# Optimization experiments

Measured on AMD Instinct MI355X. Metric: run time of the kernel, lower is better.

Reference implementation:

```python
import jax, jax.numpy as jnp
import numpy as np
import math
from itertools import combinations_with_replacement

D_KEY, D_VAL, P = 32, 64, 2
ALPHA = 1.0 / (math.factorial(P) * D_KEY ** (P / 2))  # 1/(p! * d_key^(p/2))
B, H, S = 1, 8, 512


def _make_M_C():
    # M_p: unique monomial index tuples i_1 <= ... <= i_p, shape [m_p, p]
    M = np.array(list(combinations_with_replacement(range(D_KEY), P)), dtype=np.int32)
    m_p = M.shape[0]
    counts = np.zeros((m_p, D_KEY), dtype=np.int64)
    for j in range(P):
        counts[np.arange(m_p), M[:, j]] += 1
    logfac_counts = np.vectorize(lambda v: math.lgamma(v + 1.0))(counts).sum(-1)
    C = np.round(np.exp(math.lgamma(P + 1.0) - logfac_counts)).astype(np.float32)
    return M, C


def setup_inputs() -> dict:
    key = jax.random.key(0)
    kq, kk, kv = jax.random.split(key, 3)
    M, C = _make_M_C()
    return {
        "Q": jax.random.normal(kq, (B, H, S, D_KEY), dtype=jnp.float32),
        "K": jax.random.normal(kk, (B, H, S, D_KEY), dtype=jnp.float32),
        "V": jax.random.normal(kv, (B, H, S, D_VAL), dtype=jnp.float32),
        "M": jnp.asarray(M),
        "C": jnp.asarray(C),
        "continue_prev": 0,
    }


def reference(Q, K, V, M, C, continue_prev):
    # Monomial features: Phi[b,h,s,m] = prod_j X[b,h,s,M[m,j]]
    Phi_Q = jnp.prod(Q[..., M], axis=-1)  # [B,H,S,m]
    Phi_K = jnp.prod(K[..., M], axis=-1)  # [B,H,S,m]
    # Causal prefix-sum of the Phi_K (x) V outer-product state
    H_S = jnp.cumsum(Phi_K[..., None] * V[..., None, :], axis=-3) * ALPHA  # [B,H,S,m,d_val]
    H_Z = jnp.cumsum(Phi_K, axis=-2) * ALPHA                                # [B,H,S,m] (d=1 squeezed)
    # continue_prev is False (0): no carried state to add.
    Y_S = jnp.einsum('m,bhsm,bhsmd->bhsd', C, Phi_Q, H_S)  # [B,H,S,d_val]
    Y_Z = jnp.einsum('m,bhsm,bhsm->bhs', C, Phi_Q, H_Z)[..., None]  # [B,H,S,1]
    return Y_S, Y_Z
```

## Files before the change

### kernel.cpp

```cpp
#include <hip/hip_runtime.h>
#include <hip/hip_bf16.h>


typedef __attribute__((ext_vector_type(8))) short short8;
typedef __attribute__((ext_vector_type(4))) float floatx4;

constexpr int H_ = 8, S_ = 512, DK = 32, DV = 64;
constexpr float ALPHA = 1.0f / 64.0f;

__device__ __forceinline__ unsigned int pk_bf16(float a, float b) {
    __hip_bfloat162 h = __float22bfloat162_rn(make_float2(a, b));
    union { __hip_bfloat162 h2; unsigned int u; } cvt;
    cvt.h2 = h;
    return cvt.u;
}
__device__ __forceinline__ void split8_cvt(float4 a, float4 b, short8& hi, short8& lo) {
    float f[8] = {a.x, a.y, a.z, a.w, b.x, b.y, b.z, b.w};
    unsigned int hp[4];
    hp[0] = pk_bf16(f[0], f[1]); hp[1] = pk_bf16(f[2], f[3]);
    hp[2] = pk_bf16(f[4], f[5]); hp[3] = pk_bf16(f[6], f[7]);
    float lo_f[8];
    #pragma unroll
    for (int p = 0; p < 4; ++p) {
        float he = __uint_as_float(hp[p] << 16);
        float ho = __uint_as_float(hp[p] & 0xFFFF0000u);
        lo_f[2 * p]     = f[2 * p]     - he;
        lo_f[2 * p + 1] = f[2 * p + 1] - ho;
    }
    unsigned int lp[4];
    lp[0] = pk_bf16(lo_f[0], lo_f[1]); lp[1] = pk_bf16(lo_f[2], lo_f[3]);
    lp[2] = pk_bf16(lo_f[4], lo_f[5]); lp[3] = pk_bf16(lo_f[6], lo_f[7]);
    #pragma unroll
    for (int p = 0; p < 4; ++p) {
        hi[2 * p] = (short)(hp[p] & 0xFFFF); hi[2 * p + 1] = (short)(hp[p] >> 16);
        lo[2 * p] = (short)(lp[p] & 0xFFFF); lo[2 * p + 1] = (short)(lp[p] >> 16);
    }
}

__global__ __launch_bounds__(512) void taylor_fused_v6(
    const float* __restrict__ Qg, const float* __restrict__ Kg,
    const float* __restrict__ Vg, float* __restrict__ out)
{
    const int t = threadIdx.x;
    const int c = t >> 6;
    const int l = t & 63;
    const int h = blockIdx.x & 7;
    const int qt = 15 - (blockIdx.x >> 3);
    const int qbase = qt * 32;
    const int nc = (qt >> 1) + 1;
    const int g = l >> 4, r15 = l & 15;

    __shared__ alignas(16) char Ssm[8 * 4096];
    __shared__ alignas(16) float4 Racc[8][8][64];
    __shared__ float Zb[8][32];

    floatx4 acc[2][4] = {};
    float zacc[2] = {0.f, 0.f};

    if (c < nc) {
        const bool last = (c == nc - 1);

        float4 qraw[2][2];
        #pragma unroll
        for (int qtile = 0; qtile < 2; ++qtile) {
            const float* qp = Qg + (size_t)(h * S_ + qbase + qtile * 16 + r15) * DK + g * 8;
            qraw[qtile][0] = *(const float4*)qp;
            qraw[qtile][1] = *(const float4*)(qp + 4);
        }
        float4 kraw[4][2];
        #pragma unroll
        for (int ktile = 0; ktile < 4; ++ktile) {
            const float* kp = Kg + (size_t)(h * S_ + c * 64 + ktile * 16 + r15) * DK + g * 8;
            kraw[ktile][0] = *(const float4*)kp;
            kraw[ktile][1] = *(const float4*)(kp + 4);
        }
        float vraw[2][4][8];
        #pragma unroll
        for (int kc = 0; kc < 2; ++kc)
            #pragma unroll
            for (int dtile = 0; dtile < 4; ++dtile) {
                const float* vp = Vg + (size_t)(h * S_ + c * 64 + kc * 32 + g * 8) * DV
                                     + dtile * 16 + r15;
                #pragma unroll
                for (int j = 0; j < 8; ++j)
                    vraw[kc][dtile][j] = vp[(size_t)j * DV];
            }

        short8 qBh[2], qBl[2];
        #pragma unroll
        for (int qtile = 0; qtile < 2; ++qtile)
            split8_cvt(qraw[qtile][0], qraw[qtile][1], qBh[qtile], qBl[qtile]);

        char* ssmW = Ssm + c * 4096;

        #pragma unroll
        for (int ktile = 0; ktile < 4; ++ktile) {
            short8 kAh, kAl;
            split8_cvt(kraw[ktile][0], kraw[ktile][1], kAh, kAl);
            #pragma unroll
            for (int qtile = 0; qtile < 2; ++qtile) {
                floatx4 cc_ = {0.f, 0.f, 0.f, 0.f};
                cc_ = __builtin_amdgcn_mfma_f32_16x16x32_bf16(kAh, qBh[qtile], cc_, 0, 0, 0);
                cc_ = __builtin_amdgcn_mfma_f32_16x16x32_bf16(kAh, qBl[qtile], cc_, 0, 0, 0);
                cc_ = __builtin_amdgcn_mfma_f32_16x16x32_bf16(kAl, qBh[qtile], cc_, 0, 0, 0);
                const int qg = qbase + qtile * 16 + r15;
                const int kb = c * 64 + ktile * 16 + g * 4;
                float s[4];
                #pragma unroll
                for (int rr = 0; rr < 4; ++rr) {
                    float sv = cc_[rr] * cc_[rr] * ALPHA;
                    if (last && (kb + rr > qg)) sv = 0.f;
                    s[rr] = sv;
                }
                zacc[qtile] += (s[0] + s[1]) + (s[2] + s[3]);
                unsigned int p0 = pk_bf16(s[0], s[1]);
                unsigned int p1 = pk_bf16(s[2], s[3]);
                const int qrow = qtile * 16 + r15;
                const int k0 = ktile * 16 + g * 4;
                const int byte = qrow * 128 + (((k0 >> 3) ^ (qrow & 7)) << 4) + ((k0 & 7) * 2);
                *(unsigned int*)(ssmW + byte)     = p0;
                *(unsigned int*)(ssmW + byte + 4) = p1;
            }
        }

        short8 vB[2][4];
        #pragma unroll
        for (int kc = 0; kc < 2; ++kc)
            #pragma unroll
            for (int dtile = 0; dtile < 4; ++dtile) {
                #pragma unroll
                for (int p = 0; p < 4; ++p) {
                    unsigned int pk = pk_bf16(vraw[kc][dtile][2 * p], vraw[kc][dtile][2 * p + 1]);
                    vB[kc][dtile][2 * p]     = (short)(pk & 0xFFFF);
                    vB[kc][dtile][2 * p + 1] = (short)(pk >> 16);
                }
            }

        #pragma unroll
        for (int kc = 0; kc < 2; ++kc) {
            short8 sA[2];
            #pragma unroll
            for (int qtile = 0; qtile < 2; ++qtile) {
                const int qrow = qtile * 16 + r15;
                const int g16 = kc * 4 + g;
                sA[qtile] = *(const short8*)(ssmW + qrow * 128 + ((g16 ^ (qrow & 7)) << 4));
            }
            #pragma unroll
            for (int dtile = 0; dtile < 4; ++dtile) {
                acc[0][dtile] = __builtin_amdgcn_mfma_f32_16x16x32_bf16(sA[0], vB[kc][dtile], acc[0][dtile], 0, 0, 0);
                acc[1][dtile] = __builtin_amdgcn_mfma_f32_16x16x32_bf16(sA[1], vB[kc][dtile], acc[1][dtile], 0, 0, 0);
            }
        }

        #pragma unroll
        for (int qtile = 0; qtile < 2; ++qtile) {
            float z = zacc[qtile];
            z += __shfl_xor(z, 16);
            z += __shfl_xor(z, 32);
            zacc[qtile] = z;
        }
    }

    {
        #pragma unroll
        for (int f = 0; f < 8; ++f) {
            floatx4 a = acc[f >> 2][f & 3];
            Racc[c][f][l] = make_float4(a[0], a[1], a[2], a[3]);
        }
        if (l < 32) Zb[c][l] = (l < 16) ? zacc[0] : zacc[1];
    }
    __syncthreads();

    {
        float4 sum = make_float4(0.f, 0.f, 0.f, 0.f);
        #pragma unroll
        for (int cw = 0; cw < 8; ++cw) {
            float4 v = Racc[cw][c][l];
            sum.x += v.x; sum.y += v.y; sum.z += v.z; sum.w += v.w;
        }
        const int qtile = c >> 2, dtile = c & 3;
        const int d = dtile * 16 + r15;
        float sv[4] = {sum.x, sum.y, sum.z, sum.w};
        #pragma unroll
        for (int rr = 0; rr < 4; ++rr) {
            int q = qbase + qtile * 16 + g * 4 + rr;
            out[(size_t)(h * S_ + q) * DV + d] = sv[rr];
        }
    }
    if (t < 32) {
        float z = 0.f;
        #pragma unroll
        for (int cw = 0; cw < 8; ++cw) z += Zb[cw][t];
        out[(size_t)(H_ * S_ * DV) + h * S_ + qbase + t] = z;
    }
}

extern "C" void kernel_launch(void* const* d_in, const int* in_sizes, int n_in,
                              void* d_out, int out_size, void* d_ws, size_t ws_size,
                              hipStream_t stream) {
    const float* Q = (const float*)d_in[0];
    const float* K = (const float*)d_in[1];
    const float* V = (const float*)d_in[2];
    float* out = (float*)d_out;

    taylor_fused_v6<<<128, 512, 0, stream>>>(Q, K, V, out);
}
```

Baseline: 11.29 us.

## Drop split-bf16 QK precision and split key chunks across 16 waves

Replaces the three-MFMA hi/lo split-bf16 QK^T product with a single plain bf16 MFMA, which removes the split conversion work and two thirds of the QK matrix ops. It also doubles the block to 1024 threads so each wave handles a 32-key chunk instead of 64. That shortens per-wave latency and skips the idle half-chunk on the causal diagonal. The partial results of wave pairs are combined in shared memory with an extra barrier. The risk is accuracy: squaring a bf16-rounded dot product raises the error and could break tolerance.

```diff
diff --git a/kernel.cpp b/kernel.cpp
--- a/kernel.cpp
+++ b/kernel.cpp
@@ -10,55 +10,41 @@
 
 __device__ __forceinline__ unsigned int pk_bf16(float a, float b) {
     __hip_bfloat162 h = __float22bfloat162_rn(make_float2(a, b));
-    union { __hip_bfloat162 h2; unsigned int u; } cvt;
-    cvt.h2 = h;
+    union { __hip_bfloat162 h2; unsigned int u; } cvt; cvt.h2 = h;
     return cvt.u;
 }
-__device__ __forceinline__ void split8_cvt(float4 a, float4 b, short8& hi, short8& lo) {
-    float f[8] = {a.x, a.y, a.z, a.w, b.x, b.y, b.z, b.w};
-    unsigned int hp[4];
-    hp[0] = pk_bf16(f[0], f[1]); hp[1] = pk_bf16(f[2], f[3]);
-    hp[2] = pk_bf16(f[4], f[5]); hp[3] = pk_bf16(f[6], f[7]);
-    float lo_f[8];
-    #pragma unroll
-    for (int p = 0; p < 4; ++p) {
-        float he = __uint_as_float(hp[p] << 16);
-        float ho = __uint_as_float(hp[p] & 0xFFFF0000u);
-        lo_f[2 * p]     = f[2 * p]     - he;
-        lo_f[2 * p + 1] = f[2 * p + 1] - ho;
-    }
-    unsigned int lp[4];
-    lp[0] = pk_bf16(lo_f[0], lo_f[1]); lp[1] = pk_bf16(lo_f[2], lo_f[3]);
-    lp[2] = pk_bf16(lo_f[4], lo_f[5]); lp[3] = pk_bf16(lo_f[6], lo_f[7]);
-    #pragma unroll
-    for (int p = 0; p < 4; ++p) {
-        hi[2 * p] = (short)(hp[p] & 0xFFFF); hi[2 * p + 1] = (short)(hp[p] >> 16);
-        lo[2 * p] = (short)(lp[p] & 0xFFFF); lo[2 * p + 1] = (short)(lp[p] >> 16);
-    }
+__device__ __forceinline__ short8 pack8(float4 a, float4 b) {
+    union { unsigned int u[4]; short8 s; } r;
+    r.u[0] = pk_bf16(a.x, a.y); r.u[1] = pk_bf16(a.z, a.w);
+    r.u[2] = pk_bf16(b.x, b.y); r.u[3] = pk_bf16(b.z, b.w);
+    return r.s;
 }
 
-__global__ __launch_bounds__(512) void taylor_fused_v6(
+__global__ __launch_bounds__(1024) void taylor_v7(
     const float* __restrict__ Qg, const float* __restrict__ Kg,
     const float* __restrict__ Vg, float* __restrict__ out)
 {
     const int t = threadIdx.x;
-    const int c = t >> 6;
+    const int w = t >> 6;
     const int l = t & 63;
+    const int c = w >> 1, e = w & 1;
     const int h = blockIdx.x & 7;
     const int qt = 15 - (blockIdx.x >> 3);
     const int qbase = qt * 32;
-    const int nc = (qt >> 1) + 1;
     const int g = l >> 4, r15 = l & 15;
 
-    __shared__ alignas(16) char Ssm[8 * 4096];
+    const bool active = (w <= qt);
+    const bool last   = (w == qt);
+
+    __shared__ alignas(16) char Ssm[16 * 2048];
     __shared__ alignas(16) float4 Racc[8][8][64];
-    __shared__ float Zb[8][32];
+    __shared__ float Zb[16][32];
 
     floatx4 acc[2][4] = {};
     float zacc[2] = {0.f, 0.f};
 
-    if (c < nc) {
-        const bool last = (c == nc - 1);
+    if (active) {
+        const int kb = c * 64 + e * 32;
 
         float4 qraw[2][2];
         #pragma unroll
@@ -67,90 +53,80 @@
             qraw[qtile][0] = *(const float4*)qp;
             qraw[qtile][1] = *(const float4*)(qp + 4);
         }
-        float4 kraw[4][2];
+        float4 kraw[2][2];
         #pragma unroll
-        for (int ktile = 0; ktile < 4; ++ktile) {
-            const float* kp = Kg + (size_t)(h * S_ + c * 64 + ktile * 16 + r15) * DK + g * 8;
+        for (int ktile = 0; ktile < 2; ++ktile) {
+            const float* kp = Kg + (size_t)(h * S_ + kb + ktile * 16 + r15) * DK + g * 8;
             kraw[ktile][0] = *(const float4*)kp;
             kraw[ktile][1] = *(const float4*)(kp + 4);
         }
-        float vraw[2][4][8];
+        float vraw[4][8];
         #pragma unroll
-        for (int kc = 0; kc < 2; ++kc)
+        for (int dtile = 0; dtile < 4; ++dtile) {
+            const float* vp = Vg + (size_t)(h * S_ + kb + g * 8) * DV + dtile * 16 + r15;
             #pragma unroll
-            for (int dtile = 0; dtile < 4; ++dtile) {
-                const float* vp = Vg + (size_t)(h * S_ + c * 64 + kc * 32 + g * 8) * DV
-                                     + dtile * 16 + r15;
-                #pragma unroll
-                for (int j = 0; j < 8; ++j)
-                    vraw[kc][dtile][j] = vp[(size_t)j * DV];
-            }
+            for (int j = 0; j < 8; ++j)
+                vraw[dtile][j] = vp[(size_t)j * DV];
+        }
 
-        short8 qBh[2], qBl[2];
+        short8 qB[2], kA[2];
         #pragma unroll
-        for (int qtile = 0; qtile < 2; ++qtile)
-            split8_cvt(qraw[qtile][0], qraw[qtile][1], qBh[qtile], qBl[qtile]);
+        for (int i = 0; i < 2; ++i) {
+            qB[i] = pack8(qraw[i][0], qraw[i][1]);
+            kA[i] = pack8(kraw[i][0], kraw[i][1]);
+        }
 
-        char* ssmW = Ssm + c * 4096;
+        char* ssmW = Ssm + w * 2048;
 
         #pragma unroll
-        for (int ktile = 0; ktile < 4; ++ktile) {
-            short8 kAh, kAl;
-            split8_cvt(kraw[ktile][0], kraw[ktile][1], kAh, kAl);
+        for (int ktile = 0; ktile < 2; ++ktile) {
             #pragma unroll
             for (int qtile = 0; qtile < 2; ++qtile) {
                 floatx4 cc_ = {0.f, 0.f, 0.f, 0.f};
-                cc_ = __builtin_amdgcn_mfma_f32_16x16x32_bf16(kAh, qBh[qtile], cc_, 0, 0, 0);
-                cc_ = __builtin_amdgcn_mfma_f32_16x16x32_bf16(kAh, qBl[qtile], cc_, 0, 0, 0);
-                cc_ = __builtin_amdgcn_mfma_f32_16x16x32_bf16(kAl, qBh[qtile], cc_, 0, 0, 0);
+                cc_ = __builtin_amdgcn_mfma_f32_16x16x32_bf16(kA[ktile], qB[qtile], cc_, 0, 0, 0);
                 const int qg = qbase + qtile * 16 + r15;
-                const int kb = c * 64 + ktile * 16 + g * 4;
+                const int k0 = kb + ktile * 16 + g * 4;
                 float s[4];
                 #pragma unroll
                 for (int rr = 0; rr < 4; ++rr) {
                     float sv = cc_[rr] * cc_[rr] * ALPHA;
-                    if (last && (kb + rr > qg)) sv = 0.f;
+                    if (last && (k0 + rr > qg)) sv = 0.f;
                     s[rr] = sv;
                 }
                 zacc[qtile] += (s[0] + s[1]) + (s[2] + s[3]);
                 unsigned int p0 = pk_bf16(s[0], s[1]);
                 unsigned int p1 = pk_bf16(s[2], s[3]);
                 const int qrow = qtile * 16 + r15;
-                const int k0 = ktile * 16 + g * 4;
-                const int byte = qrow * 128 + (((k0 >> 3) ^ (qrow & 7)) << 4) + ((k0 & 7) * 2);
-                *(unsigned int*)(ssmW + byte)     = p0;
-                *(unsigned int*)(ssmW + byte + 4) = p1;
+                const int swz = (qrow ^ (qrow >> 2)) & 3;
+                const int gi = ktile * 2 + (g >> 1);
+                const int byte = qrow * 64 + ((gi ^ swz) << 4) + (g & 1) * 8;
+                *(uint2*)(ssmW + byte) = make_uint2(p0, p1);
             }
         }
 
-        short8 vB[2][4];
+        short8 vB[4];
         #pragma unroll
-        for (int kc = 0; kc < 2; ++kc)
+        for (int dtile = 0; dtile < 4; ++dtile) {
+            union { unsigned int u[4]; short8 s; } r;
             #pragma unroll
-            for (int dtile = 0; dtile < 4; ++dtile) {
-                #pragma unroll
-                for (int p = 0; p < 4; ++p) {
-                    unsigned int pk = pk_bf16(vraw[kc][dtile][2 * p], vraw[kc][dtile][2 * p + 1]);
-                    vB[kc][dtile][2 * p]     = (short)(pk & 0xFFFF);
-                    vB[kc][dtile][2 * p + 1] = (short)(pk >> 16);
-                }
-            }
+            for (int p = 0; p < 4; ++p)
+                r.u[p] = pk_bf16(vraw[dtile][2 * p], vraw[dtile][2 * p + 1]);
+            vB[dtile] = r.s;
+        }
 
+        short8 sA[2];
         #pragma unroll
-        for (int kc = 0; kc < 2; ++kc) {
-            short8 sA[2];
+        for (int qtile = 0; qtile < 2; ++qtile) {
+            const int qrow = qtile * 16 + r15;
+            const int swz = (qrow ^ (qrow >> 2)) & 3;
+            sA[qtile] = *(const short8*)(ssmW + qrow * 64 + ((g ^ swz) << 4));
+        }
+        #pragma unroll
+        for (int qtile = 0; qtile < 2; ++qtile)
             #pragma unroll
-            for (int qtile = 0; qtile < 2; ++qtile) {
-                const int qrow = qtile * 16 + r15;
-                const int g16 = kc * 4 + g;
-                sA[qtile] = *(const short8*)(ssmW + qrow * 128 + ((g16 ^ (qrow & 7)) << 4));
-            }
-            #pragma unroll
-            for (int dtile = 0; dtile < 4; ++dtile) {
-                acc[0][dtile] = __builtin_amdgcn_mfma_f32_16x16x32_bf16(sA[0], vB[kc][dtile], acc[0][dtile], 0, 0, 0);
-                acc[1][dtile] = __builtin_amdgcn_mfma_f32_16x16x32_bf16(sA[1], vB[kc][dtile], acc[1][dtile], 0, 0, 0);
-            }
-        }
+            for (int dtile = 0; dtile < 4; ++dtile)
+                acc[qtile][dtile] = __builtin_amdgcn_mfma_f32_16x16x32_bf16(
+                    sA[qtile], vB[dtile], acc[qtile][dtile], 0, 0, 0);
 
         #pragma unroll
         for (int qtile = 0; qtile < 2; ++qtile) {
@@ -161,24 +137,34 @@
         }
     }
 
-    {
+    if (e == 1) {
         #pragma unroll
         for (int f = 0; f < 8; ++f) {
             floatx4 a = acc[f >> 2][f & 3];
             Racc[c][f][l] = make_float4(a[0], a[1], a[2], a[3]);
         }
-        if (l < 32) Zb[c][l] = (l < 16) ? zacc[0] : zacc[1];
+    }
+    if (l < 32) Zb[w][l] = (l < 16) ? zacc[0] : zacc[1];
+    __syncthreads();
+
+    if (e == 0) {
+        #pragma unroll
+        for (int f = 0; f < 8; ++f) {
+            float4 p = Racc[c][f][l];
+            floatx4 a = acc[f >> 2][f & 3];
+            Racc[c][f][l] = make_float4(a[0] + p.x, a[1] + p.y, a[2] + p.z, a[3] + p.w);
+        }
     }
     __syncthreads();
 
-    {
+    if (w < 8) {
         float4 sum = make_float4(0.f, 0.f, 0.f, 0.f);
         #pragma unroll
         for (int cw = 0; cw < 8; ++cw) {
-            float4 v = Racc[cw][c][l];
+            float4 v = Racc[cw][w][l];
             sum.x += v.x; sum.y += v.y; sum.z += v.z; sum.w += v.w;
         }
-        const int qtile = c >> 2, dtile = c & 3;
+        const int qtile = w >> 2, dtile = w & 3;
         const int d = dtile * 16 + r15;
         float sv[4] = {sum.x, sum.y, sum.z, sum.w};
         #pragma unroll
@@ -190,7 +176,7 @@
     if (t < 32) {
         float z = 0.f;
         #pragma unroll
-        for (int cw = 0; cw < 8; ++cw) z += Zb[cw][t];
+        for (int ww = 0; ww < 16; ++ww) z += Zb[ww][t];
         out[(size_t)(H_ * S_ * DV) + h * S_ + qbase + t] = z;
     }
 }
@@ -203,5 +189,5 @@
     const float* V = (const float*)d_in[2];
     float* out = (float*)d_out;
 
-    taylor_fused_v6<<<128, 512, 0, stream>>>(Q, K, V, out);
+    taylor_v7<<<128, 1024, 0, stream>>>(Q, K, V, out);
 }
```

Measured after the change: 12.83 us. 1.14x slower.
